# Optimization experiments

Measured on AMD Instinct MI355X. Metric: run time of the kernel, lower is better.

The kernel has to match this reference:

```python
import jax, jax.numpy as jnp
import numpy as np

D_MODEL = 256
GAMMA = 0.9          # ret_D is built in the torch forward but never applied to the output; kept for fidelity notes
SCALE_BASE = 512     # XPOS default
TEMP = 10000.0
TWO_PI = 2.0 * np.pi


def sine_pos_embed(x):
    """DETR-style 1D sine position embedding with an all-ones mask (as in forward).
    x: [B,T,C] -> pos: [1,T,C] (mask is [1,T] ones, so batch dim broadcasts)."""
    T, C = x.shape[1], x.shape[2]
    x_embed = jnp.arange(1, T + 1, dtype=jnp.float32)          # cumsum of ones
    x_embed = x_embed / (x_embed[-1] + 1e-6) * TWO_PI          # normalize=True
    dim_t = TEMP ** (2.0 * (jnp.arange(C) // 2).astype(jnp.float32) / C)
    pos = x_embed[:, None] / dim_t                             # [T,C]
    pos = jnp.stack([jnp.sin(pos[:, 0::2]), jnp.cos(pos[:, 1::2])], axis=2).reshape(T, C)
    return pos[None].astype(x.dtype)


def _dup_interleave(m):
    # [L, d/2] -> [L, d], columns repeated pairwise: [a,b] -> [a,a,b,b]
    return jnp.repeat(m, 2, axis=-1)


def _rotate_every_two(x):
    x1, x2 = x[..., 0::2], x[..., 1::2]
    return jnp.stack([-x2, x1], axis=-1).reshape(x.shape)


def xpos_apply(x, downscale=False):
    """RetNet XPOS rotary embedding. x: [B,L,d]."""
    L, d = x.shape[1], x.shape[2]
    half = d // 2
    scale_vec = (jnp.arange(0, d, 2, dtype=jnp.float32) + 0.4 * d) / (1.4 * d)   # [d/2]
    power = jnp.arange(L, dtype=jnp.float32) / SCALE_BASE
    scale = scale_vec[None, :] ** power[:, None]                                  # [L, d/2]
    inv_freq = 1.0 / (TEMP ** (jnp.arange(half, dtype=jnp.float32) / half))
    sinusoid = jnp.arange(L, dtype=jnp.float32)[:, None] * inv_freq[None, :]      # [L, d/2]
    sin, cos = jnp.sin(sinusoid), jnp.cos(sinusoid)
    if downscale:
        scale = 1.0 / scale
    sin_s = _dup_interleave(sin * scale)[None].astype(x.dtype)   # [1,L,d]
    cos_s = _dup_interleave(cos * scale)[None].astype(x.dtype)
    return x * cos_s + _rotate_every_two(x) * sin_s


def setup_inputs() -> dict:
    key = jax.random.key(0)
    ks = jax.random.split(key, 8)
    B, TXT, VID, D = 16, 32, 2048, D_MODEL
    S = TXT + VID
    inp = {
        "src": jax.random.normal(ks[0], (B, S, D), dtype=jnp.float32),
        "learn_vid_ret": jax.random.normal(ks[1], (VID * VID, 1), dtype=jnp.float32),
        "W_txt_Q": jax.random.normal(ks[2], (D, D), dtype=jnp.float32) / D,
        "W_txt_K": jax.random.normal(ks[3], (D, D), dtype=jnp.float32) / D,
        "W_txt_V": jax.random.normal(ks[4], (D, D), dtype=jnp.float32) / D,
        "W_vid_Q": jax.random.normal(ks[5], (D, D), dtype=jnp.float32) / D,
        "W_vid_K": jax.random.normal(ks[6], (D, D), dtype=jnp.float32) / D,
        "W_vid_V": jax.random.normal(ks[7], (D, D), dtype=jnp.float32) / D,
        "txt_length": TXT,
    }
    return inp


def reference(src, learn_vid_ret, W_txt_Q, W_txt_K, W_txt_V, W_vid_Q, W_vid_K, W_vid_V, txt_length):
    S = src.shape[1]
    vid_length = S - txt_length

    # learned retention mask over the video block
    learn_ret = jax.nn.sigmoid(learn_vid_ret.reshape(vid_length, vid_length))
    diag = jnp.eye(vid_length, dtype=src.dtype)
    video_ret = (1.0 - diag) * learn_ret
    loss_sparsity = jnp.mean(jnp.abs(video_ret))

    # full [S,S] mask: ones everywhere, sigmoid(learned) on the vid-vid block
    ret_mask = jnp.ones((S, S), dtype=src.dtype).at[txt_length:, txt_length:].set(learn_ret)

    txt_mem = src[:, :txt_length]   # [B,TXT,D]
    vid_mem = src[:, txt_length:]   # [B,VID,D]

    pos = sine_pos_embed(txt_mem)   # [1,TXT,D]
    txt_Q = (pos + txt_mem) @ W_txt_Q
    txt_K = (pos + txt_mem) @ W_txt_K
    vid_Q = xpos_apply(vid_mem @ W_vid_Q)
    vid_K = xpos_apply(vid_mem @ W_vid_K, downscale=True)

    Q = jnp.concatenate([txt_Q, vid_Q], axis=1)                  # [B,S,D]
    K = jnp.concatenate([txt_K, vid_K], axis=1)                  # [B,S,D]
    V = jnp.concatenate([txt_mem @ W_txt_V, vid_mem @ W_vid_V], axis=1)

    # retention: QK^T elementwise-masked (no softmax), then weighted V sum
    scores = jnp.einsum('bsd,btd->bst', Q, K) * ret_mask[None]   # [B,S,S]
    out = scores @ V                                             # [B,S,D]
    return out, loss_sparsity
```

## Files before the change

### kernel.cpp

```cpp
#include <hip/hip_runtime.h>

#define B_   16
#define TXT  32
#define VID  2048
#define D_   256
#define S_   2080
#define SP   2176
#define NKT  34
#define GTOT 17424

typedef unsigned short ushort_t;
typedef __attribute__((ext_vector_type(8))) short short8;
typedef __attribute__((ext_vector_type(4))) short short4v;
typedef __attribute__((ext_vector_type(4))) float f32x4;
typedef __attribute__((ext_vector_type(16))) float f32x16;

__device__ __forceinline__ ushort_t f2bf(float f) {
  unsigned u = __builtin_bit_cast(unsigned, f);
  unsigned r = (u + 0x7FFFu + ((u >> 16) & 1u)) >> 16;
  return (ushort_t)r;
}
__device__ __forceinline__ float bf2f(ushort_t h) {
  unsigned u = ((unsigned)h) << 16;
  return __builtin_bit_cast(float, u);
}

__device__ __forceinline__ void g2l16(void* lds, const void* g) {
  __builtin_amdgcn_global_load_lds(
      (const __attribute__((address_space(1))) char*)g,
      (__attribute__((address_space(3))) char*)lds, 16, 0, 0);
}

__device__ __forceinline__ f32x4 mfma16(short8 a, short8 b, f32x4 c) {
  return __builtin_amdgcn_mfma_f32_16x16x32_bf16(a, b, c, 0, 0, 0);
}
__device__ __forceinline__ f32x16 mfma32(short8 a, short8 b, f32x16 c) {
  return __builtin_amdgcn_mfma_f32_32x32x16_bf16(a, b, c, 0, 0, 0);
}


__global__ void prep_kernel(const float* __restrict__ src, const float* __restrict__ learn,
                            const float* __restrict__ Wtq, const float* __restrict__ Wtk,
                            const float* __restrict__ Wtv,
                            const float* __restrict__ Wvq, const float* __restrict__ Wvk,
                            const float* __restrict__ Wvv,
                            ushort_t* __restrict__ Qs, ushort_t* __restrict__ Ks,
                            ushort_t* __restrict__ VTs, ushort_t* __restrict__ sigp,
                            float* __restrict__ tbl, ushort_t* __restrict__ WT,
                            float* __restrict__ loss) {
  __shared__ float shf[64 * 68];
  const int blk = blockIdx.x;
  const int tid = threadIdx.x;

  if (blk < 64) {
    float (*a_s)[256] = (float(*)[256])shf;
    float (*x_s)[256] = (float(*)[256])(shf + 2048);
    const int tg = blk & 3;
    const int b  = blk >> 2;
    const int c  = tid;
    #pragma unroll
    for (int t = 0; t < 8; ++t) {
      int row = tg * 8 + t;
      float x = src[((size_t)b * S_ + row) * D_ + c];
      float xe = (float)(row + 1) * (6.283185307179586f / (32.0f + 1e-6f));
      int i = c >> 1;
      float dimt = powf(10000.0f, (2.0f * (float)i) / 256.0f);
      float ang = xe / dimt;
      float pv = (c & 1) ? cosf(ang) : sinf(ang);
      x_s[t][c] = x;
      a_s[t][c] = x + pv;
    }
    __syncthreads();
    float q[8] = {0,0,0,0,0,0,0,0}, k[8] = {0,0,0,0,0,0,0,0}, v[8] = {0,0,0,0,0,0,0,0};
    for (int kk = 0; kk < 256; ++kk) {
      float wq = Wtq[(size_t)kk * 256 + c];
      float wk = Wtk[(size_t)kk * 256 + c];
      float wv = Wtv[(size_t)kk * 256 + c];
      #pragma unroll
      for (int t = 0; t < 8; ++t) {
        q[t] = fmaf(a_s[t][kk], wq, q[t]);
        k[t] = fmaf(a_s[t][kk], wk, k[t]);
        v[t] = fmaf(x_s[t][kk], wv, v[t]);
      }
    }
    #pragma unroll
    for (int t = 0; t < 8; ++t) {
      int row = tg * 8 + t;
      size_t base = ((size_t)(b * NKT)) << 14;
      size_t sub = (size_t)(c >> 4) * 1024 + row * 16 + (c & 15);
      Qs[base + sub] = f2bf(q[t]);
      Ks[base + sub] = f2bf(k[t]);
      VTs[base + (size_t)(row >> 4) * 4096 + c * 16 + (row & 15)] = f2bf(v[t]);
    }
  } else if (blk < 112) {
    float (*t)[68] = (float(*)[68])shf;
    const int m = blk - 64;
    const int k0 = (m & 3) * 64, n0 = ((m >> 2) & 3) * 64, mt = m >> 4;
    const float* W = (mt == 0) ? Wvq : (mt == 1) ? Wvk : Wvv;
    int r = tid >> 4, cq = (tid & 15) * 4;
    #pragma unroll
    for (int mm = 0; mm < 4; ++mm) {
      int k = mm * 16 + r;
      float4 v = *(const float4*)(W + (size_t)(k0 + k) * 256 + n0 + cq);
      t[k][cq] = v.x; t[k][cq + 1] = v.y; t[k][cq + 2] = v.z; t[k][cq + 3] = v.w;
    }
    __syncthreads();
    #pragma unroll
    for (int mm = 0; mm < 4; ++mm) {
      int n = mm * 16 + r;
      short4v h;
      h[0] = (short)f2bf(t[cq + 0][n]);
      h[1] = (short)f2bf(t[cq + 1][n]);
      h[2] = (short)f2bf(t[cq + 2][n]);
      h[3] = (short)f2bf(t[cq + 3][n]);
      *(short4v*)(WT + ((size_t)mt * D_ + n0 + n) * D_ + k0 + cq) = h;
    }
  } else if (blk < 1136) {
    int idx = (blk - 112) * 256 + tid;
    int n = idx >> 7, i = idx & 127;
    float invf = powf(10000.0f, -(float)i / 128.0f);
    float ang = (float)n * invf;
    float s, co;
    sincosf(ang, &s, &co);
    float sv = ((float)(2 * i) + 102.4f) / 358.4f;
    float sc = powf(sv, (float)n / 512.0f);
    float4 r;
    r.x = co * sc; r.y = s * sc; r.z = co / sc; r.w = s / sc;
    *(float4*)(tbl + (size_t)idx * 4) = r;
  } else if (blk < 1328) {
    int i = (blk - 1136) * 256 + tid;
    short8 z = {0, 0, 0, 0, 0, 0, 0, 0};
    int sec = i >> 14;
    int j = i & 16383;
    int bb = j >> 10;
    int rem = j & 1023;
    size_t base = ((size_t)(bb * NKT + 32)) << 14;
    if (sec == 0) {
      int kstep = rem >> 6, ch = rem & 63;
      *(short8*)(Qs + base + kstep * 1024 + 512 + ch * 8) = z;
    } else if (sec == 1) {
      int kstep = rem >> 6, ch = rem & 63;
      *(short8*)(Ks + base + kstep * 1024 + 512 + ch * 8) = z;
    } else {
      *(short8*)(VTs + base + 8192 + rem * 8) = z;
    }
  } else {
    float* red = shf;
    const int base = ((blk - 1328) * 256 + tid) * 8;
    float4 v0 = *(const float4*)(learn + base);
    float4 v1 = *(const float4*)(learn + base + 4);
    float vals[8] = {v0.x, v0.y, v0.z, v0.w, v1.x, v1.y, v1.z, v1.w};
    float acc = 0.f;
    short8 sh;
    #pragma unroll
    for (int j = 0; j < 8; ++j) {
      int idx = base + j;
      float s = 1.0f / (1.0f + expf(-vals[j]));
      sh[j] = (short)f2bf(s);
      int rr = idx >> 11, cc = idx & 2047;
      if (rr != cc) acc += s;
    }
    *(short8*)(sigp + base) = sh;
    red[tid] = acc;
    __syncthreads();
    #pragma unroll
    for (int st = 128; st > 0; st >>= 1) {
      if (tid < st) red[tid] += red[tid + st];
      __syncthreads();
    }
    if (tid == 0) atomicAdd(loss, red[0] * (1.0f / 4194304.0f));
  }
}

__global__ __launch_bounds__(256, 2) void vid_gemm(
    const float* __restrict__ src, const ushort_t* __restrict__ WT,
    const float* __restrict__ tbl,
    ushort_t* __restrict__ Qs, ushort_t* __restrict__ Ks, ushort_t* __restrict__ VTs) {
  __shared__ __align__(16) ushort_t ldsA[64 * 256];
  __shared__ __align__(16) ushort_t ldsB[64 * 64];

  const int rt = blockIdx.x;
  const int b  = blockIdx.y;
  const int tid = threadIdx.x;
  const int wv = tid >> 6, lane = tid & 63, l15 = lane & 15, l4 = lane >> 4;

  #pragma unroll
  for (int m = 0; m < 16; ++m) {
    int idx = m * 256 + tid;
    int r = idx >> 6;
    int c4 = (idx & 63) * 4;
    const float4 v = *(const float4*)(src + ((size_t)b * S_ + TXT + rt * 64 + r) * D_ + c4);
    short4v h;
    h[0] = (short)f2bf(v.x); h[1] = (short)f2bf(v.y);
    h[2] = (short)f2bf(v.z); h[3] = (short)f2bf(v.w);
    int off = ((r << 9) + (c4 << 1)) ^ ((r & 7) << 4);
    *(short4v*)((char*)ldsA + off) = h;
  }
  __syncthreads();

  for (int ct = 0; ct < 12; ++ct) {
    const int nt = ct >> 2;
    const int n0 = (ct & 3) * 64;

    f32x4 acc[4];
    #pragma unroll
    for (int t2 = 0; t2 < 4; ++t2) { acc[t2][0] = 0.f; acc[t2][1] = 0.f; acc[t2][2] = 0.f; acc[t2][3] = 0.f; }

    for (int k4 = 0; k4 < 4; ++k4) {
      const int kk = k4 * 64;
      #pragma unroll
      for (int m = 0; m < 2; ++m) {
        int p = (m * 256 + tid) * 16;
        int nl = p >> 7;
        int c = (p & 127) ^ ((nl & 7) << 4);
        g2l16((char*)ldsB + p, (const char*)(WT + ((size_t)nt * D_ + n0 + nl) * D_ + kk) + c);
      }
      __syncthreads();
      #pragma unroll
      for (int ks = 0; ks < 2; ++ks) {
        int ar = wv * 16 + l15;
        int aoff = ((ar << 9) + ((kk + ks * 32 + l4 * 8) << 1)) ^ ((ar & 7) << 4);
        short8 av = *(const short8*)((const char*)ldsA + aoff);
        #pragma unroll
        for (int t2 = 0; t2 < 4; ++t2) {
          int nl = t2 * 16 + l15;
          int boff = ((nl << 7) + ((ks * 32 + l4 * 8) << 1)) ^ ((nl & 7) << 4);
          short8 bv = *(const short8*)((const char*)ldsB + boff);
          acc[t2] = mfma16(av, bv, acc[t2]);
        }
      }
      __syncthreads();
    }

    const int rowl = wv * 16 + l4 * 4;
    if (nt < 2) {
      #pragma unroll
      for (int t2 = 0; t2 < 4; ++t2) {
        int c = n0 + t2 * 16 + l15;
        #pragma unroll
        for (int r = 0; r < 4; ++r) {
          int n = rt * 64 + rowl + r;
          float x = acc[t2][r];
          float xp = __shfl_xor(x, 1);
          const float4 tb = *(const float4*)(tbl + ((size_t)n * 128 + (c >> 1)) * 4);
          float cs = (nt == 0) ? tb.x : tb.z;
          float ss = (nt == 0) ? tb.y : tb.w;
          float val = (c & 1) ? fmaf(x, cs, xp * ss) : fmaf(x, cs, -xp * ss);
          int rowg = TXT + n;
          size_t idx = (((size_t)(b * NKT + (rowg >> 6))) << 14)
                     + (size_t)(c >> 4) * 1024 + (rowg & 63) * 16 + (c & 15);
          if (nt == 0) Qs[idx] = f2bf(val);
          else         Ks[idx] = f2bf(val);
        }
      }
    } else {
      #pragma unroll
      for (int t2 = 0; t2 < 4; ++t2)
        #pragma unroll
        for (int r = 0; r < 4; ++r) {
          int rr = rowl + r;
          int cc = t2 * 16 + l15;
          int off = ((rr << 7) + (cc << 1)) ^ ((rr & 7) << 4);
          *(ushort_t*)((char*)ldsB + off) = f2bf(acc[t2][r]);
        }
      __syncthreads();
      int n = tid >> 2;
      int rc = (tid & 3) * 16;
      short8 o0, o1;
      #pragma unroll
      for (int j = 0; j < 8; ++j) {
        int rr = rc + j;
        int off = ((rr << 7) + (n << 1)) ^ ((rr & 7) << 4);
        o0[j] = *(const short*)((const char*)ldsB + off);
      }
      #pragma unroll
      for (int j = 0; j < 8; ++j) {
        int rr = rc + 8 + j;
        int off = ((rr << 7) + (n << 1)) ^ ((rr & 7) << 4);
        o1[j] = *(const short*)((const char*)ldsB + off);
      }
      int d = n0 + n;
      int kvg0 = TXT + rt * 64 + rc;
      size_t base = (((size_t)(b * NKT + (kvg0 >> 6))) << 14) + ((kvg0 >> 4) & 3) * 4096 + d * 16;
      *(short8*)(VTs + base) = o0;
      *(short8*)(VTs + base + 8) = o1;
      __syncthreads();
    }
  }
}

__global__ __launch_bounds__(256, 2) void attn_kernel(
    const ushort_t* __restrict__ Qs, const ushort_t* __restrict__ Ks,
    const ushort_t* __restrict__ VTs, const ushort_t* __restrict__ sigp,
    float* __restrict__ out) {
  __shared__ __align__(16) ushort_t Kb[16384];
  __shared__ __align__(16) ushort_t Vb[16384];
  __shared__ __align__(16) ushort_t Pb[4096];

  const int kblk = blockIdx.x;
  const int bs = (kblk & 7) * 64 + (kblk >> 3);
  int g = bs * 34 + (bs >> 5);
  const int gend = (bs + 1) * 34 + ((bs + 1) >> 5);

  const int tid = threadIdx.x;
  const int wid = tid >> 6, lane = tid & 63;
  const int l31 = lane & 31, l5 = lane >> 5;
  const int qh = wid >> 1, kh = wid & 1;
  const int d0 = wid * 64;
  const int qloc = qh * 32 + l31;
  const int pswz = (l31 & 7) << 4;

  int b = g / 1089, rem = g - b * 1089, qt = rem / 33, kvt = rem - qt * 33;

  short8 qf[16];
  int4 mq[4];

  auto ldq = [&](int bb, int qq) {
    const ushort_t* qb = Qs + (((size_t)(bb * NKT + qq)) << 14) + qloc * 16 + l5 * 8;
    #pragma unroll
    for (int ks = 0; ks < 16; ++ks) qf[ks] = *(const short8*)(qb + ks * 1024);
  };
  auto ldmask = [&](int qq, int tt) {
    int q = qq * 64 + qloc;
    int qc = q - TXT; qc = qc < 0 ? 0 : (qc > 2047 ? 2047 : qc);
    int kvp = tt * 64 + kh * 32 - TXT;
    int kvc = (kvp >= 0 && kvp <= 2016) ? kvp : 0;
    const int4* mrow = (const int4*)(sigp + (size_t)qc * 2048 + kvc);
    mq[0] = mrow[0]; mq[1] = mrow[1]; mq[2] = mrow[2]; mq[3] = mrow[3];
  };
  auto stageK = [&](int bb, int tt) {
    const char* src = (const char*)Ks + (((size_t)(bb * NKT + tt)) << 15);
    #pragma unroll
    for (int m = 0; m < 8; ++m) { int s2 = m * 256 + tid; g2l16((char*)Kb + s2 * 16, src + s2 * 16); }
  };
  auto stageV = [&](int bb, int tt) {
    const char* src = (const char*)VTs + (((size_t)(bb * NKT + tt)) << 15);
    #pragma unroll
    for (int m = 0; m < 8; ++m) { int s2 = m * 256 + tid; g2l16((char*)Vb + s2 * 16, src + s2 * 16); }
  };

  f32x16 oacc[2][2];
  #pragma unroll
  for (int i2 = 0; i2 < 2; ++i2)
    #pragma unroll
    for (int j2 = 0; j2 < 2; ++j2)
      #pragma unroll
      for (int r = 0; r < 16; ++r) oacc[i2][j2][r] = 0.f;

  auto flushO = [&](int bb, int qq) {
    #pragma unroll
    for (int qg2 = 0; qg2 < 2; ++qg2)
      #pragma unroll
      for (int dg = 0; dg < 2; ++dg)
        #pragma unroll
        for (int r = 0; r < 16; ++r) {
          int qg = qq * 64 + qg2 * 32 + (r & 3) + 8 * (r >> 2) + 4 * l5;
          int dd = d0 + dg * 32 + l31;
          if (qg < S_)
            unsafeAtomicAdd(&out[((size_t)bb * S_ + qg) * D_ + dd], oacc[qg2][dg][r]);
          oacc[qg2][dg][r] = 0.f;
        }
  };

  stageK(b, kvt);
  ldmask(qt, kvt);
  stageV(b, kvt);
  ldq(b, qt);
  asm volatile("s_waitcnt vmcnt(0)" ::: "memory");
  __builtin_amdgcn_sched_barrier(0);
  __builtin_amdgcn_s_barrier();
  __builtin_amdgcn_sched_barrier(0);

  while (g < gend) {
    int gn = (g + 1 < GTOT) ? g + 1 : GTOT - 1;
    int nb = gn / 1089, nrem = gn - nb * 1089, nqt = nrem / 33, nkvt = nrem - nqt * 33;

    f32x16 s0, s1;
    #pragma unroll
    for (int r = 0; r < 16; ++r) { s0[r] = 0.f; s1[r] = 0.f; }
    const int arow = (kh * 32 + l31) * 32 + l5 * 16;
    __builtin_amdgcn_s_setprio(1);
    #pragma unroll
    for (int ks = 0; ks < 8; ++ks) {
      short8 ka = *(const short8*)((const char*)Kb + ks * 2048 + arow);
      short8 kc = *(const short8*)((const char*)Kb + (ks + 8) * 2048 + arow);
      s0 = mfma32(ka, qf[ks], s0);
      s1 = mfma32(kc, qf[ks + 8], s1);
    }
    __builtin_amdgcn_s_setprio(0);

    {
      int q = qt * 64 + qloc;
      bool qv = (q >= TXT) && (q < S_);
      int kvp = kvt * 64 + kh * 32 - TXT;
      bool kvv = (kvp >= 0 && kvp <= 2016);
      bool ok = qv && kvv;
      const unsigned* mw = (const unsigned*)mq;
      #pragma unroll
      for (int t = 0; t < 4; ++t) {
        unsigned w0p, w1p;
        {
          unsigned wa = mw[4 * t + 0], wb = mw[4 * t + 2];
          unsigned w = l5 ? wb : wa;
          float m0 = ok ? bf2f((ushort_t)(w & 0xFFFFu)) : 1.0f;
          float m1 = ok ? bf2f((ushort_t)(w >> 16)) : 1.0f;
          int r = 4 * t;
          float p0 = (s0[r] + s1[r]) * m0;
          float p1 = (s0[r + 1] + s1[r + 1]) * m1;
          asm("v_cvt_pk_bf16_f32 %0, %1, %2" : "=v"(w0p) : "v"(p0), "v"(p1));
        }
        {
          unsigned wa = mw[4 * t + 1], wb = mw[4 * t + 3];
          unsigned w = l5 ? wb : wa;
          float m0 = ok ? bf2f((ushort_t)(w & 0xFFFFu)) : 1.0f;
          float m1 = ok ? bf2f((ushort_t)(w >> 16)) : 1.0f;
          int r = 4 * t + 2;
          float p0 = (s0[r] + s1[r]) * m0;
          float p1 = (s0[r + 1] + s1[r + 1]) * m1;
          asm("v_cvt_pk_bf16_f32 %0, %1, %2" : "=v"(w1p) : "v"(p0), "v"(p1));
        }
        int off = ((qloc << 7) + (kh << 6) + (t << 4) + (l5 << 3)) ^ pswz;
        *(uint2*)((char*)Pb + off) = make_uint2(w0p, w1p);
      }
    }

    asm volatile("s_waitcnt vmcnt(0) lgkmcnt(0)" ::: "memory");
    __builtin_amdgcn_sched_barrier(0);
    __builtin_amdgcn_s_barrier();
    __builtin_amdgcn_sched_barrier(0);

    stageK(nb, nkvt);
    __builtin_amdgcn_sched_barrier(0);

    __builtin_amdgcn_s_setprio(1);
    #pragma unroll
    for (int ks = 0; ks < 4; ++ks) {
      int p0 = (l31 * 128 + ks * 32 + l5 * 16) ^ pswz;
      int p1 = ((32 + l31) * 128 + ks * 32 + l5 * 16) ^ pswz;
      short8 pf0 = *(const short8*)((const char*)Pb + p0);
      short8 pf1 = *(const short8*)((const char*)Pb + p1);
      short8 vf0 = *(const short8*)((const char*)Vb + ks * 8192 + (d0 + l31) * 32 + l5 * 16);
      short8 vf1 = *(const short8*)((const char*)Vb + ks * 8192 + (d0 + 32 + l31) * 32 + l5 * 16);
      oacc[0][0] = mfma32(pf0, vf0, oacc[0][0]);
      oacc[0][1] = mfma32(pf0, vf1, oacc[0][1]);
      oacc[1][0] = mfma32(pf1, vf0, oacc[1][0]);
      oacc[1][1] = mfma32(pf1, vf1, oacc[1][1]);
    }
    __builtin_amdgcn_s_setprio(0);
    asm volatile("s_waitcnt lgkmcnt(0)" ::: "memory");
    __builtin_amdgcn_sched_barrier(0);
    __builtin_amdgcn_s_barrier();
    __builtin_amdgcn_sched_barrier(0);

    ldmask(nqt, nkvt);
    __builtin_amdgcn_sched_barrier(0);
    const bool qchange = (nqt != qt || nb != b);
    if (qchange) {
      flushO(b, qt);
      ldq(nb, nqt);
    }
    __builtin_amdgcn_sched_barrier(0);
    stageV(nb, nkvt);
    __builtin_amdgcn_sched_barrier(0);
    if (qchange) { asm volatile("s_waitcnt vmcnt(24)" ::: "memory"); }
    else         { asm volatile("s_waitcnt vmcnt(12)" ::: "memory"); }
    __builtin_amdgcn_sched_barrier(0);
    __builtin_amdgcn_s_barrier();
    __builtin_amdgcn_sched_barrier(0);

    b = nb; qt = nqt; kvt = nkvt; ++g;
  }

  flushO(b, qt);
}

extern "C" void kernel_launch(void* const* d_in, const int* in_sizes, int n_in,
                              void* d_out, int out_size, void* d_ws, size_t ws_size,
                              hipStream_t stream) {
  (void)in_sizes; (void)n_in; (void)ws_size;
  const float* src   = (const float*)d_in[0];
  const float* learn = (const float*)d_in[1];
  const float* Wtq = (const float*)d_in[2];
  const float* Wtk = (const float*)d_in[3];
  const float* Wtv = (const float*)d_in[4];
  const float* Wvq = (const float*)d_in[5];
  const float* Wvk = (const float*)d_in[6];
  const float* Wvv = (const float*)d_in[7];
  float* out = (float*)d_out;

  char* ws = (char*)d_ws;
  const size_t QKV_ONE  = (size_t)B_ * SP * D_ * 2;
  const size_t QP_OFF   = 0;
  const size_t KS_OFF   = QP_OFF + QKV_ONE;
  const size_t VT_OFF   = KS_OFF + QKV_ONE;
  const size_t SIG_OFF  = VT_OFF + QKV_ONE;
  const size_t TBL_OFF  = SIG_OFF + (size_t)VID * VID * 2;
  const size_t WT_OFF   = TBL_OFF + (size_t)VID * 128 * 4 * sizeof(float);

  ushort_t* Qs   = (ushort_t*)(ws + QP_OFF);
  ushort_t* Ks   = (ushort_t*)(ws + KS_OFF);
  ushort_t* VTs  = (ushort_t*)(ws + VT_OFF);
  ushort_t* sigp = (ushort_t*)(ws + SIG_OFF);
  float*    tbl  = (float*)(ws + TBL_OFF);
  ushort_t* WT   = (ushort_t*)(ws + WT_OFF);
  float*    loss = out + (size_t)B_ * S_ * D_;

  hipMemsetAsync(d_out, 0, (size_t)out_size * sizeof(float), stream);
  prep_kernel<<<3376, 256, 0, stream>>>(src, learn, Wtq, Wtk, Wtv, Wvq, Wvk, Wvv,
                                        Qs, Ks, VTs, sigp, tbl, WT, loss);
  vid_gemm<<<dim3(32, B_), 256, 0, stream>>>(src, WT, tbl, Qs, Ks, VTs);
  attn_kernel<<<dim3(512), 256, 0, stream>>>(Qs, Ks, VTs, sigp, out);
}
```

Baseline: 316.6 us.

## Split vid_gemm over output column tiles, pre-convert src to bf16, reswizzle P buffer

Moves vid_gemm's 12 output column tiles from a serial loop onto a third grid dimension, so 6144 blocks run instead of 512 and the A-operand LDS tile shrinks to 64x64. When the workspace is large enough, a separate kernel first converts the video part of src to bf16 so the GEMM can stream A with async global-to-LDS copies. The attention kernel's P buffer layout and XOR swizzle are also changed, likely to cut LDS bank conflicts. The cost is that each column tile re-reads A, plus an extra launch and an extra pass over src.

```diff
diff --git a/kernel.cpp b/kernel.cpp
--- a/kernel.cpp
+++ b/kernel.cpp
@@ -172,120 +172,140 @@
   }
 }
 
+__global__ void cvt_kernel(const float* __restrict__ src, ushort_t* __restrict__ srcb) {
+  int i = blockIdx.x * 256 + threadIdx.x;
+  int b = i >> 16;
+  int rem = i & 65535;
+  int row = rem >> 5, c8 = (rem & 31) * 8;
+  const float* p = src + ((size_t)b * S_ + TXT + row) * D_ + c8;
+  float4 v0 = *(const float4*)p;
+  float4 v1 = *(const float4*)(p + 4);
+  short8 h;
+  h[0] = (short)f2bf(v0.x); h[1] = (short)f2bf(v0.y); h[2] = (short)f2bf(v0.z); h[3] = (short)f2bf(v0.w);
+  h[4] = (short)f2bf(v1.x); h[5] = (short)f2bf(v1.y); h[6] = (short)f2bf(v1.z); h[7] = (short)f2bf(v1.w);
+  *(short8*)(srcb + ((size_t)b * VID + row) * D_ + c8) = h;
+}
+
+template <int MODE>
 __global__ __launch_bounds__(256, 2) void vid_gemm(
-    const float* __restrict__ src, const ushort_t* __restrict__ WT,
-    const float* __restrict__ tbl,
+    const float* __restrict__ src, const ushort_t* __restrict__ srcb,
+    const ushort_t* __restrict__ WT, const float* __restrict__ tbl,
     ushort_t* __restrict__ Qs, ushort_t* __restrict__ Ks, ushort_t* __restrict__ VTs) {
-  __shared__ __align__(16) ushort_t ldsA[64 * 256];
+  __shared__ __align__(16) ushort_t ldsA[64 * 64];
   __shared__ __align__(16) ushort_t ldsB[64 * 64];
 
   const int rt = blockIdx.x;
   const int b  = blockIdx.y;
+  const int ct = blockIdx.z;
+  const int nt = ct >> 2;
+  const int n0 = (ct & 3) * 64;
   const int tid = threadIdx.x;
   const int wv = tid >> 6, lane = tid & 63, l15 = lane & 15, l4 = lane >> 4;
 
+  f32x4 acc[4];
   #pragma unroll
-  for (int m = 0; m < 16; ++m) {
-    int idx = m * 256 + tid;
-    int r = idx >> 6;
-    int c4 = (idx & 63) * 4;
-    const float4 v = *(const float4*)(src + ((size_t)b * S_ + TXT + rt * 64 + r) * D_ + c4);
-    short4v h;
-    h[0] = (short)f2bf(v.x); h[1] = (short)f2bf(v.y);
-    h[2] = (short)f2bf(v.z); h[3] = (short)f2bf(v.w);
-    int off = ((r << 9) + (c4 << 1)) ^ ((r & 7) << 4);
-    *(short4v*)((char*)ldsA + off) = h;
-  }
-  __syncthreads();
-
-  for (int ct = 0; ct < 12; ++ct) {
-    const int nt = ct >> 2;
-    const int n0 = (ct & 3) * 64;
-
-    f32x4 acc[4];
-    #pragma unroll
-    for (int t2 = 0; t2 < 4; ++t2) { acc[t2][0] = 0.f; acc[t2][1] = 0.f; acc[t2][2] = 0.f; acc[t2][3] = 0.f; }
-
-    for (int k4 = 0; k4 < 4; ++k4) {
-      const int kk = k4 * 64;
+  for (int t2 = 0; t2 < 4; ++t2) { acc[t2][0] = 0.f; acc[t2][1] = 0.f; acc[t2][2] = 0.f; acc[t2][3] = 0.f; }
+
+  for (int kk = 0; kk < 256; kk += 64) {
+    if (MODE == 1) {
       #pragma unroll
       for (int m = 0; m < 2; ++m) {
         int p = (m * 256 + tid) * 16;
-        int nl = p >> 7;
-        int c = (p & 127) ^ ((nl & 7) << 4);
-        g2l16((char*)ldsB + p, (const char*)(WT + ((size_t)nt * D_ + n0 + nl) * D_ + kk) + c);
-      }
-      __syncthreads();
-      #pragma unroll
-      for (int ks = 0; ks < 2; ++ks) {
-        int ar = wv * 16 + l15;
-        int aoff = ((ar << 9) + ((kk + ks * 32 + l4 * 8) << 1)) ^ ((ar & 7) << 4);
-        short8 av = *(const short8*)((const char*)ldsA + aoff);
-        #pragma unroll
-        for (int t2 = 0; t2 < 4; ++t2) {
-          int nl = t2 * 16 + l15;
-          int boff = ((nl << 7) + ((ks * 32 + l4 * 8) << 1)) ^ ((nl & 7) << 4);
-          short8 bv = *(const short8*)((const char*)ldsB + boff);
-          acc[t2] = mfma16(av, bv, acc[t2]);
-        }
-      }
-      __syncthreads();
-    }
-
-    const int rowl = wv * 16 + l4 * 4;
-    if (nt < 2) {
+        int r = p >> 7;
+        int cb = (p & 127) ^ ((r & 7) << 4);
+        g2l16((char*)ldsA + p,
+              (const char*)(srcb + ((size_t)b * VID + rt * 64 + r) * D_ + kk) + cb);
+      }
+    } else {
+      #pragma unroll
+      for (int m = 0; m < 4; ++m) {
+        int q = m * 256 + tid;
+        int r = q >> 4;
+        int kc = (q & 15) * 4;
+        const float4 v = *(const float4*)(src + ((size_t)b * S_ + TXT + rt * 64 + r) * D_ + kk + kc);
+        short4v h;
+        h[0] = (short)f2bf(v.x); h[1] = (short)f2bf(v.y);
+        h[2] = (short)f2bf(v.z); h[3] = (short)f2bf(v.w);
+        int off = ((r << 7) + (kc << 1)) ^ ((r & 7) << 4);
+        *(short4v*)((char*)ldsA + off) = h;
+      }
+    }
+    #pragma unroll
+    for (int m = 0; m < 2; ++m) {
+      int p = (m * 256 + tid) * 16;
+      int nl = p >> 7;
+      int c = (p & 127) ^ ((nl & 7) << 4);
+      g2l16((char*)ldsB + p, (const char*)(WT + ((size_t)nt * D_ + n0 + nl) * D_ + kk) + c);
+    }
+    __syncthreads();
+    #pragma unroll
+    for (int ks = 0; ks < 2; ++ks) {
+      int ar = wv * 16 + l15;
+      int aoff = ((ar << 7) + ((ks * 32 + l4 * 8) << 1)) ^ ((ar & 7) << 4);
+      short8 av = *(const short8*)((const char*)ldsA + aoff);
       #pragma unroll
       for (int t2 = 0; t2 < 4; ++t2) {
-        int c = n0 + t2 * 16 + l15;
-        #pragma unroll
-        for (int r = 0; r < 4; ++r) {
-          int n = rt * 64 + rowl + r;
-          float x = acc[t2][r];
-          float xp = __shfl_xor(x, 1);
-          const float4 tb = *(const float4*)(tbl + ((size_t)n * 128 + (c >> 1)) * 4);
-          float cs = (nt == 0) ? tb.x : tb.z;
-          float ss = (nt == 0) ? tb.y : tb.w;
-          float val = (c & 1) ? fmaf(x, cs, xp * ss) : fmaf(x, cs, -xp * ss);
-          int rowg = TXT + n;
-          size_t idx = (((size_t)(b * NKT + (rowg >> 6))) << 14)
-                     + (size_t)(c >> 4) * 1024 + (rowg & 63) * 16 + (c & 15);
-          if (nt == 0) Qs[idx] = f2bf(val);
-          else         Ks[idx] = f2bf(val);
-        }
-      }
-    } else {
-      #pragma unroll
-      for (int t2 = 0; t2 < 4; ++t2)
-        #pragma unroll
-        for (int r = 0; r < 4; ++r) {
-          int rr = rowl + r;
-          int cc = t2 * 16 + l15;
-          int off = ((rr << 7) + (cc << 1)) ^ ((rr & 7) << 4);
-          *(ushort_t*)((char*)ldsB + off) = f2bf(acc[t2][r]);
-        }
-      __syncthreads();
-      int n = tid >> 2;
-      int rc = (tid & 3) * 16;
-      short8 o0, o1;
-      #pragma unroll
-      for (int j = 0; j < 8; ++j) {
-        int rr = rc + j;
-        int off = ((rr << 7) + (n << 1)) ^ ((rr & 7) << 4);
-        o0[j] = *(const short*)((const char*)ldsB + off);
-      }
-      #pragma unroll
-      for (int j = 0; j < 8; ++j) {
-        int rr = rc + 8 + j;
-        int off = ((rr << 7) + (n << 1)) ^ ((rr & 7) << 4);
-        o1[j] = *(const short*)((const char*)ldsB + off);
-      }
-      int d = n0 + n;
-      int kvg0 = TXT + rt * 64 + rc;
-      size_t base = (((size_t)(b * NKT + (kvg0 >> 6))) << 14) + ((kvg0 >> 4) & 3) * 4096 + d * 16;
-      *(short8*)(VTs + base) = o0;
-      *(short8*)(VTs + base + 8) = o1;
-      __syncthreads();
-    }
+        int nl = t2 * 16 + l15;
+        int boff = ((nl << 7) + ((ks * 32 + l4 * 8) << 1)) ^ ((nl & 7) << 4);
+        short8 bv = *(const short8*)((const char*)ldsB + boff);
+        acc[t2] = mfma16(av, bv, acc[t2]);
+      }
+    }
+    __syncthreads();
+  }
+
+  const int rowl = wv * 16 + l4 * 4;
+  if (nt < 2) {
+    #pragma unroll
+    for (int t2 = 0; t2 < 4; ++t2) {
+      int c = n0 + t2 * 16 + l15;
+      #pragma unroll
+      for (int r = 0; r < 4; ++r) {
+        int n = rt * 64 + rowl + r;
+        float x = acc[t2][r];
+        float xp = __shfl_xor(x, 1);
+        const float4 tb = *(const float4*)(tbl + ((size_t)n * 128 + (c >> 1)) * 4);
+        float cs = (nt == 0) ? tb.x : tb.z;
+        float ss = (nt == 0) ? tb.y : tb.w;
+        float val = (c & 1) ? fmaf(x, cs, xp * ss) : fmaf(x, cs, -xp * ss);
+        int rowg = TXT + n;
+        size_t idx = (((size_t)(b * NKT + (rowg >> 6))) << 14)
+                   + (size_t)(c >> 4) * 1024 + (rowg & 63) * 16 + (c & 15);
+        if (nt == 0) Qs[idx] = f2bf(val);
+        else         Ks[idx] = f2bf(val);
+      }
+    }
+  } else {
+    #pragma unroll
+    for (int t2 = 0; t2 < 4; ++t2)
+      #pragma unroll
+      for (int r = 0; r < 4; ++r) {
+        int rr = rowl + r;
+        int cc = t2 * 16 + l15;
+        int off = ((rr << 7) + (cc << 1)) ^ ((rr & 7) << 4);
+        *(ushort_t*)((char*)ldsA + off) = f2bf(acc[t2][r]);
+      }
+    __syncthreads();
+    int n = tid >> 2;
+    int rc = (tid & 3) * 16;
+    short8 o0, o1;
+    #pragma unroll
+    for (int j = 0; j < 8; ++j) {
+      int rr = rc + j;
+      int off = ((rr << 7) + (n << 1)) ^ ((rr & 7) << 4);
+      o0[j] = *(const short*)((const char*)ldsA + off);
+    }
+    #pragma unroll
+    for (int j = 0; j < 8; ++j) {
+      int rr = rc + 8 + j;
+      int off = ((rr << 7) + (n << 1)) ^ ((rr & 7) << 4);
+      o1[j] = *(const short*)((const char*)ldsA + off);
+    }
+    int d = n0 + n;
+    int kvg0 = TXT + rt * 64 + rc;
+    size_t base = (((size_t)(b * NKT + (kvg0 >> 6))) << 14) + ((kvg0 >> 4) & 3) * 4096 + d * 16;
+    *(short8*)(VTs + base) = o0;
+    *(short8*)(VTs + base + 8) = o1;
   }
 }
 
@@ -308,7 +328,7 @@
   const int qh = wid >> 1, kh = wid & 1;
   const int d0 = wid * 64;
   const int qloc = qh * 32 + l31;
-  const int pswz = (l31 & 7) << 4;
+  const int pkey = (l31 & 15) << 4;
 
   int b = g / 1089, rem = g - b * 1089, qt = rem / 33, kvt = rem - qt * 33;
 
@@ -419,7 +439,7 @@
           float p1 = (s0[r + 1] + s1[r + 1]) * m1;
           asm("v_cvt_pk_bf16_f32 %0, %1, %2" : "=v"(w1p) : "v"(p0), "v"(p1));
         }
-        int off = ((qloc << 7) + (kh << 6) + (t << 4) + (l5 << 3)) ^ pswz;
+        int off = (l31 << 8) + (((qh << 7) + (kh << 6) + (t << 4) + (l5 << 3)) ^ pkey);
         *(uint2*)((char*)Pb + off) = make_uint2(w0p, w1p);
       }
     }
@@ -435,8 +455,8 @@
     __builtin_amdgcn_s_setprio(1);
     #pragma unroll
     for (int ks = 0; ks < 4; ++ks) {
-      int p0 = (l31 * 128 + ks * 32 + l5 * 16) ^ pswz;
-      int p1 = ((32 + l31) * 128 + ks * 32 + l5 * 16) ^ pswz;
+      int p0 = (l31 << 8) + ((ks * 32 + l5 * 16) ^ pkey);
+      int p1 = (l31 << 8) + ((128 + ks * 32 + l5 * 16) ^ pkey);
       short8 pf0 = *(const short8*)((const char*)Pb + p0);
       short8 pf1 = *(const short8*)((const char*)Pb + p1);
       short8 vf0 = *(const short8*)((const char*)Vb + ks * 8192 + (d0 + l31) * 32 + l5 * 16);
@@ -477,7 +497,7 @@
 extern "C" void kernel_launch(void* const* d_in, const int* in_sizes, int n_in,
                               void* d_out, int out_size, void* d_ws, size_t ws_size,
                               hipStream_t stream) {
-  (void)in_sizes; (void)n_in; (void)ws_size;
+  (void)in_sizes; (void)n_in;
   const float* src   = (const float*)d_in[0];
   const float* learn = (const float*)d_in[1];
   const float* Wtq = (const float*)d_in[2];
@@ -496,6 +516,8 @@
   const size_t SIG_OFF  = VT_OFF + QKV_ONE;
   const size_t TBL_OFF  = SIG_OFF + (size_t)VID * VID * 2;
   const size_t WT_OFF   = TBL_OFF + (size_t)VID * 128 * 4 * sizeof(float);
+  const size_t SRCB_OFF = WT_OFF + (size_t)3 * D_ * D_ * 2;
+  const size_t NEED_SRCB = SRCB_OFF + (size_t)B_ * VID * D_ * 2;
 
   ushort_t* Qs   = (ushort_t*)(ws + QP_OFF);
   ushort_t* Ks   = (ushort_t*)(ws + KS_OFF);
@@ -503,11 +525,17 @@
   ushort_t* sigp = (ushort_t*)(ws + SIG_OFF);
   float*    tbl  = (float*)(ws + TBL_OFF);
   ushort_t* WT   = (ushort_t*)(ws + WT_OFF);
+  ushort_t* srcb = (ushort_t*)(ws + SRCB_OFF);
   float*    loss = out + (size_t)B_ * S_ * D_;
 
   hipMemsetAsync(d_out, 0, (size_t)out_size * sizeof(float), stream);
   prep_kernel<<<3376, 256, 0, stream>>>(src, learn, Wtq, Wtk, Wtv, Wvq, Wvk, Wvv,
                                         Qs, Ks, VTs, sigp, tbl, WT, loss);
-  vid_gemm<<<dim3(32, B_), 256, 0, stream>>>(src, WT, tbl, Qs, Ks, VTs);
+  if (ws_size >= NEED_SRCB) {
+    cvt_kernel<<<4096, 256, 0, stream>>>(src, srcb);
+    vid_gemm<1><<<dim3(32, B_, 12), 256, 0, stream>>>(src, srcb, WT, tbl, Qs, Ks, VTs);
+  } else {
+    vid_gemm<0><<<dim3(32, B_, 12), 256, 0, stream>>>(src, srcb, WT, tbl, Qs, Ks, VTs);
+  }
   attn_kernel<<<dim3(512), 256, 0, stream>>>(Qs, Ks, VTs, sigp, out);
 }
```

After: 289.7 us. 8.5% less time.
